# Performance work log

Measured on AMD Instinct MI355X. Metric: run time of the kernel, lower is better.

## Reference

```python
import jax, jax.numpy as jnp
import numpy as np

B, H, IN, OUT, T = 1024, 1024, 512, 8192, 15
EPS = 1e-5


def setup_inputs() -> dict:
    key = jax.random.key(0)
    ks = jax.random.split(key, 20)
    s = 0.02
    d = {
        'z': jax.random.normal(ks[0], (B, H), jnp.float32),
        'input_length': T,
        # ConvTranspose1d weights, torch layout [in, out, k] == jax 'IOH'
        'cw1': jax.random.normal(ks[1], (H, H, 3), jnp.float32) * s,
        'cb1': jax.random.normal(ks[2], (H,), jnp.float32) * s,
        'cw2': jax.random.normal(ks[3], (H, H, 3), jnp.float32) * s,
        'cb2': jax.random.normal(ks[4], (H,), jnp.float32) * s,
        'cw3': jax.random.normal(ks[5], (H, H, 3), jnp.float32) * s,
        'cb3': jax.random.normal(ks[6], (H,), jnp.float32) * s,
        # BatchNorm1d (eval mode: running stats)
        'bn1_g': jnp.ones((H,), jnp.float32), 'bn1_b': jnp.zeros((H,), jnp.float32),
        'bn1_m': jax.random.normal(ks[7], (H,), jnp.float32) * 0.1,
        'bn1_v': jax.random.uniform(ks[8], (H,), jnp.float32, 0.5, 1.5),
        'bn2_g': jnp.ones((H,), jnp.float32), 'bn2_b': jnp.zeros((H,), jnp.float32),
        'bn2_m': jax.random.normal(ks[9], (H,), jnp.float32) * 0.1,
        'bn2_v': jax.random.uniform(ks[10], (H,), jnp.float32, 0.5, 1.5),
        # GRUCell: weight_ih [3H, IN+H], weight_hh [3H, H]
        'w_ih': jax.random.normal(ks[11], (3 * H, IN + H), jnp.float32) * s,
        'w_hh': jax.random.normal(ks[12], (3 * H, H), jnp.float32) * s,
        'b_ih': jax.random.normal(ks[13], (3 * H,), jnp.float32) * s,
        'b_hh': jax.random.normal(ks[14], (3 * H,), jnp.float32) * s,
        # Linears (torch layout [out_features, in_features])
        'h2x_w': jax.random.normal(ks[15], (IN, H), jnp.float32) * s,
        'h2x_b': jax.random.normal(ks[16], (IN,), jnp.float32) * s,
        'dec2out_w': jax.random.normal(ks[17], (OUT, H), jnp.float32) * s,
        'dec2out_b': jnp.zeros((OUT,), jnp.float32),
        'out_w': jax.random.normal(ks[18], (OUT, H), jnp.float32) * s,
        'out_b': jnp.zeros((OUT,), jnp.float32),
    }
    return d


def _conv_t(x, w, b):
    # x: [B, C, L] ; torch ConvTranspose1d(k=3, s=2, pad=0): out L -> 2L+1
    y = jax.lax.conv_transpose(x, w, strides=(2,), padding='VALID',
                               dimension_numbers=('NCH', 'IOH', 'NCH'),
                               transpose_kernel=True)
    return y + b[None, :, None]


def _bn(x, g, bta, m, v):
    inv = g / jnp.sqrt(v + EPS)
    return (x - m[None, :, None]) * inv[None, :, None] + bta[None, :, None]


def reference(z, input_length, cw1, cb1, cw2, cb2, cw3, cb3,
              bn1_g, bn1_b, bn1_m, bn1_v, bn2_g, bn2_b, bn2_m, bn2_v,
              w_ih, w_hh, b_ih, b_hh, h2x_w, h2x_b,
              dec2out_w, dec2out_b, out_w, out_b):
    b = z.shape[0]
    # conv-transpose context: [B, H, 1] -> [B, H, 15]
    dec = z[:, :, None]
    dec = _bn(jax.nn.elu(_conv_t(dec, cw1, cb1)), bn1_g, bn1_b, bn1_m, bn1_v)
    dec = _bn(jax.nn.elu(_conv_t(dec, cw2, cb2)), bn2_g, bn2_b, bn2_m, bn2_v)
    dec = _conv_t(dec, cw3, cb3)
    dec_tbh = jnp.transpose(dec, (2, 0, 1))[:input_length]  # [T, B, H]

    inp0 = jnp.full((b, IN), float(OUT - 2), z.dtype)

    def step(carry, dec_t):
        h, inp = carry
        x = jnp.concatenate([inp, dec_t], axis=1)         # [B, IN+H]
        gi = x @ w_ih.T + b_ih
        gh = h @ w_hh.T + b_hh
        ir, iz, inn = jnp.split(gi, 3, axis=1)
        hr, hz, hn = jnp.split(gh, 3, axis=1)
        r = jax.nn.sigmoid(ir + hr)
        zg = jax.nn.sigmoid(iz + hz)
        n = jnp.tanh(inn + r * hn)
        h_new = (1.0 - zg) * n + zg * h
        inp_new = jax.nn.relu(h_new @ h2x_w.T + h2x_b)    # eval-mode branch
        return (h_new, inp_new), h_new

    (_, _), hs = jax.lax.scan(step, (z, inp0), dec_tbh)   # hs: [T, B, H]

    dec_flat = dec_tbh.reshape(-1, H)
    out_flat = hs.reshape(-1, H)
    dec_o = dec_flat @ dec2out_w.T + dec2out_b            # [T*B, OUT]
    output = out_flat @ out_w.T + out_b                   # [T*B, OUT]
    return output, dec_o
```

## Files before the change

kernel.cpp:

```cpp
#include <hip/hip_runtime.h>
#include <math.h>


#define HD    1024
#define BATCH 1024
#define IND   512
#define OUTD  8192
#define TSTEPS 15
#define EPSV  1e-5f

typedef unsigned short u16;
typedef __attribute__((ext_vector_type(8))) short bf16x8;
typedef __attribute__((ext_vector_type(8))) unsigned short u16x8;
typedef __attribute__((ext_vector_type(4))) unsigned short u16x4;
typedef __attribute__((ext_vector_type(4))) float f32x4;

__device__ __forceinline__ u16 f2b(float f) {
    union { float f; unsigned u; } x; x.f = f;
    unsigned r = x.u + 0x7fffu + ((x.u >> 16) & 1u);
    return (u16)(r >> 16);
}
__device__ __forceinline__ float b2f(u16 v) {
    union { unsigned u; float f; } x; x.u = ((unsigned)v) << 16; return x.f;
}

typedef __attribute__((address_space(1))) const void gas_t;
typedef __attribute__((address_space(3))) void las_t;
__device__ __forceinline__ void gload_lds16(const u16* g, u16* l) {
    __builtin_amdgcn_global_load_lds((gas_t*)g, (las_t*)l, 16, 0, 0);
}

template<int EPI, bool WF32, bool WB16>
__device__ __forceinline__ void gemm_tile128(
    u16* As, u16* Bs,
    int bm, int bn,
    int K1, const u16* A1, int lda1, const u16* B1, int ldb1,
    int K2, const u16* A2, int lda2, const u16* B2, int ldb2,
    const float* bias,
    const float* bng, const float* bnb, const float* bnm, const float* bnv,
    float* Cf, u16* Cb, int ldc)
{
    const int tid  = threadIdx.x;
    const int lane = tid & 63;
    const int w    = tid >> 6;
    const int wr   = w >> 1, wc = w & 1;
    const int r_in = lane >> 2;
    const int c_in = (lane & 3) * 8;

    f32x4 acc[4][4];
#pragma unroll
    for (int m = 0; m < 4; ++m)
#pragma unroll
        for (int n = 0; n < 4; ++n) acc[m][n] = (f32x4){0.f, 0.f, 0.f, 0.f};

#pragma unroll 1
    for (int pair = 0; pair < 2; ++pair) {
        const int K = pair ? K2 : K1;
        if (K == 0) continue;
        const int lda = pair ? lda2 : lda1;
        const int ldb = pair ? ldb2 : ldb1;
        const u16* Ag = (pair ? A2 : A1) + (size_t)bm * lda;
        const u16* Bg = (pair ? B2 : B1) + (size_t)bn * ldb;

        for (int k0 = 0; k0 < K; k0 += 32) {
#pragma unroll
            for (int i = 0; i < 2; ++i) {
                gload_lds16(Ag + (size_t)(i * 64 + w * 16 + r_in) * lda + k0 + c_in,
                            &As[i * 2048 + w * 512]);
                gload_lds16(Bg + (size_t)(i * 64 + w * 16 + r_in) * ldb + k0 + c_in,
                            &Bs[i * 2048 + w * 512]);
            }
            __syncthreads();

            const int fr = lane & 15;
            const int fk = (lane >> 4) * 8;
            bf16x8 av[4], bv[4];
#pragma unroll
            for (int m = 0; m < 4; ++m)
                av[m] = *(const bf16x8*)&As[(wr * 64 + m * 16 + fr) * 32 + fk];
#pragma unroll
            for (int n = 0; n < 4; ++n)
                bv[n] = *(const bf16x8*)&Bs[(wc * 64 + n * 16 + fr) * 32 + fk];
#pragma unroll
            for (int m = 0; m < 4; ++m)
#pragma unroll
                for (int n = 0; n < 4; ++n)
                    acc[m][n] = __builtin_amdgcn_mfma_f32_16x16x32_bf16(
                                    av[m], bv[n], acc[m][n], 0, 0, 0);
            __syncthreads();
        }
    }

    const int col_l = lane & 15;
    const int row_h = (lane >> 4) * 4;
#pragma unroll
    for (int m = 0; m < 4; ++m) {
#pragma unroll
        for (int j = 0; j < 4; ++j) {
            const int row = bm + wr * 64 + m * 16 + row_h + j;
#pragma unroll
            for (int n = 0; n < 4; ++n) {
                const int col = bn + wc * 64 + n * 16 + col_l;
                float v = acc[m][n][j] + bias[col];
                if (EPI == 1) {
                    float e = v > 0.f ? v : expm1f(v);
                    float sc = bng[col] * rsqrtf(bnv[col] + EPSV);
                    v = (e - bnm[col]) * sc + bnb[col];
                }
                if (WF32) Cf[(size_t)row * ldc + col] = v;
                if (WB16) Cb[(size_t)row * ldc + col] = f2b(v);
            }
        }
    }
}

__device__ __forceinline__ void proj_rider(u16* sm, int g,
    const u16* A, const u16* B, const float* bias, float* C)
{
    gemm_tile128<0, true, false>(sm, sm + 4096,
        (g >> 6) * 128, (g & 63) * 128,
        HD, A, HD, B, HD, 0, nullptr, 0, nullptr, 0,
        bias, nullptr, nullptr, nullptr, nullptr, C, nullptr, OUTD);
}

template<int EPI>
__launch_bounds__(256)
__global__ void conv_gemm(int Lin, const u16* X, const u16* W, const float* bias,
                          const float* bng, const float* bnb, const float* bnm, const float* bnv,
                          u16* Y)
{
    __shared__ __align__(16) u16 sm[8192];
    const int t = blockIdx.z;
    int l0 = 0, k0 = 0, l1 = 0, k1 = 0, cnt = 0;
    for (int l = 0; l < Lin; ++l) {
        int k = t - 2 * l;
        if (k >= 0 && k < 3) { if (!cnt) { l0 = l; k0 = k; } else { l1 = l; k1 = k; } ++cnt; }
    }
    const size_t BH = (size_t)BATCH * HD, HH = (size_t)HD * HD;
    gemm_tile128<EPI, false, true>(sm, sm + 4096,
        blockIdx.y * 128, blockIdx.x * 128,
        HD, X + l0 * BH, HD, W + k0 * HH, HD,
        cnt > 1 ? HD : 0, X + l1 * BH, HD, W + k1 * HH, HD,
        bias, bng, bnb, bnm, bnv, nullptr, Y + (size_t)t * BH, HD);
}

__launch_bounds__(512, 2)
__global__ void gemm256(int nbn, int nk,
    const u16* __restrict__ A, const u16* __restrict__ B,
    const float* __restrict__ bias, u16* __restrict__ Cb,
    int lda, int ldb, int ldc)
{
    const int nwg = gridDim.x;
    const int q = nwg >> 3, r = nwg & 7;
    const int xcd = blockIdx.x & 7, idx = blockIdx.x >> 3;
    const int wg = (xcd < r ? xcd * (q + 1) : r * (q + 1) + (xcd - r) * q) + idx;
    int bm, bn;
    const int nbm = nwg / nbn;
    if ((nbn & 3) == 0 && (nbm & 1) == 0) {
        const int nsc = nbn >> 2;
        const int super = wg >> 3, inner = wg & 7;
        const int sr = super / nsc, sc = super - sr * nsc;
        bm = (sr * 2 + (inner >> 2)) * 256;
        bn = (sc * 4 + (inner & 3)) * 256;
    } else {
        bm = (wg / nbn) * 256;
        bn = (wg % nbn) * 256;
    }

    __shared__ __align__(16) u16 smem[2][2][256 * 64];
    u16 (*As)[256 * 64] = smem[0];
    u16 (*Bs)[256 * 64] = smem[1];

    const int tid = threadIdx.x;
    const int w = tid >> 6, l = tid & 63;
    const int wr = w >> 2, wc = w & 3;
    const int srow = l >> 3;
    const int scb  = (l & 7) ^ srow;
    const int fr = l & 15, fcb = l >> 4, swz = l & 7;

    const u16* Ag = A + (size_t)bm * lda;
    const u16* Bg = B + (size_t)bn * ldb;

    auto stage = [&](int b, int kt) {
        const int k0 = kt * 64 + scb * 8;
#pragma unroll
        for (int rr = 0; rr < 4; ++rr)
            gload_lds16(Ag + (size_t)(rr * 64 + w * 8 + srow) * lda + k0,
                        &As[b][(rr * 64 + w * 8) * 64]);
#pragma unroll
        for (int rr = 0; rr < 4; ++rr)
            gload_lds16(Bg + (size_t)(rr * 64 + w * 8 + srow) * ldb + k0,
                        &Bs[b][(rr * 64 + w * 8) * 64]);
    };

    f32x4 acc[8][4];
#pragma unroll
    for (int m = 0; m < 8; ++m)
#pragma unroll
        for (int n = 0; n < 4; ++n) acc[m][n] = (f32x4){0.f, 0.f, 0.f, 0.f};

    stage(0, 0);
    asm volatile("s_waitcnt vmcnt(0)" ::: "memory");
    asm volatile("s_barrier" ::: "memory");

    for (int kt = 0; kt < nk; ++kt) {
        const int c = kt & 1;
        if (kt + 1 < nk) stage(c ^ 1, kt + 1);
#pragma unroll
        for (int ks = 0; ks < 2; ++ks) {
            bf16x8 av[8], bv[4];
#pragma unroll
            for (int m = 0; m < 8; ++m)
                av[m] = *(const bf16x8*)&As[c][
                    (wr * 128 + m * 16 + fr) * 64 + (((ks * 4 + fcb) ^ swz) * 8)];
#pragma unroll
            for (int n = 0; n < 4; ++n)
                bv[n] = *(const bf16x8*)&Bs[c][
                    (wc * 64 + n * 16 + fr) * 64 + (((ks * 4 + fcb) ^ swz) * 8)];
            __builtin_amdgcn_s_setprio(1);
#pragma unroll
            for (int m = 0; m < 8; ++m)
#pragma unroll
                for (int n = 0; n < 4; ++n)
                    acc[m][n] = __builtin_amdgcn_mfma_f32_16x16x32_bf16(
                                    av[m], bv[n], acc[m][n], 0, 0, 0);
            __builtin_amdgcn_s_setprio(0);
        }
        asm volatile("s_waitcnt vmcnt(0)" ::: "memory");
        asm volatile("s_barrier" ::: "memory");
    }

    float* fsm = (float*)smem;
    const int row_h = (l >> 4) * 4;
#pragma unroll 1
    for (int hh = 0; hh < 2; ++hh) {
        __syncthreads();
        if (wr == hh) {
#pragma unroll
            for (int m = 0; m < 8; ++m)
#pragma unroll
                for (int j = 0; j < 4; ++j) {
                    const int rl = m * 16 + row_h + j;
#pragma unroll
                    for (int n = 0; n < 4; ++n)
                        fsm[rl * 256 + wc * 64 + n * 16 + fr] = acc[m][n][j];
                }
        }
        __syncthreads();
#pragma unroll
        for (int it = 0; it < 16; ++it) {
            const int fid = it * 512 + tid;
            const int rl = fid >> 6;
            const int cf = (fid & 63) * 4;
            float4 v = *(const float4*)&fsm[rl * 256 + cf];
            v.x += bias[bn + cf + 0];
            v.y += bias[bn + cf + 1];
            v.z += bias[bn + cf + 2];
            v.w += bias[bn + cf + 3];
            u16x4 o;
            o[0] = f2b(v.x); o[1] = f2b(v.y); o[2] = f2b(v.z); o[3] = f2b(v.w);
            *(u16x4*)&Cb[(size_t)(bm + hh * 128 + rl) * ldc + bn + cf] = o;
        }
    }
}

#define KTILE(Ag, lda_, Bg, ldb_, k0_, ACC2)                                      \
  {                                                                               \
    const int k0 = (k0_);                                                         \
    gload_lds16((Ag) + (size_t)(tid >> 2) * (lda_) + k0 + (tid & 3) * 8,          \
                &As[tid * 8]);                                                    \
    _Pragma("unroll")                                                             \
    for (int i_ = 0; i_ < 3; ++i_) {                                              \
      const int u_ = tid + i_ * 256;                                              \
      gload_lds16((Bg) + (size_t)((u_ >> 8) * HD + bn + ((u_ & 255) >> 2)) * (ldb_)\
                       + k0 + (u_ & 3) * 8,                                       \
                  &Bs[u_ * 8]);                                                   \
    }                                                                             \
    __syncthreads();                                                              \
    {                                                                             \
      bf16x8 av0 = *(const bf16x8*)&As[(wr * 32 + fr) * 32 + fk];                 \
      bf16x8 av1 = *(const bf16x8*)&As[(wr * 32 + 16 + fr) * 32 + fk];            \
      _Pragma("unroll")                                                           \
      for (int n_ = 0; n_ < 2; ++n_) {                                            \
        const int bo = (wc * 32 + n_ * 16 + fr) * 32 + fk;                        \
        bf16x8 bv = *(const bf16x8*)&Bs[bo];                                      \
        ar[0][n_] = __builtin_amdgcn_mfma_f32_16x16x32_bf16(av0, bv, ar[0][n_], 0, 0, 0); \
        ar[1][n_] = __builtin_amdgcn_mfma_f32_16x16x32_bf16(av1, bv, ar[1][n_], 0, 0, 0); \
        bv = *(const bf16x8*)&Bs[2048 + bo];                                      \
        az[0][n_] = __builtin_amdgcn_mfma_f32_16x16x32_bf16(av0, bv, az[0][n_], 0, 0, 0); \
        az[1][n_] = __builtin_amdgcn_mfma_f32_16x16x32_bf16(av1, bv, az[1][n_], 0, 0, 0); \
        bv = *(const bf16x8*)&Bs[4096 + bo];                                      \
        ACC2[0][n_] = __builtin_amdgcn_mfma_f32_16x16x32_bf16(av0, bv, ACC2[0][n_], 0, 0, 0); \
        ACC2[1][n_] = __builtin_amdgcn_mfma_f32_16x16x32_bf16(av1, bv, ACC2[1][n_], 0, 0, 0); \
      }                                                                           \
    }                                                                             \
    __syncthreads();                                                              \
  }

__launch_bounds__(256)
__global__ void gih_cell(int t,
    const u16* __restrict__ inpb,  const u16* __restrict__ wih,
    const u16* __restrict__ hbp,   const u16* __restrict__ whh,
    const u16* __restrict__ gdect, const float* __restrict__ extra0,
    const float* __restrict__ b_hh, const float* __restrict__ hp,
    float* __restrict__ hf, u16* __restrict__ hsbt,
    const u16* __restrict__ dec3b, const u16* __restrict__ d2owb,
    const float* __restrict__ d2ob, float* __restrict__ out1)
{
    __shared__ __align__(16) u16 sm[8192];
    const int bid = blockIdx.x;
    const int tid = threadIdx.x, l = tid & 63, w = tid >> 6;
    const int wr = w >> 1, wc = w & 1;
    const int fr = l & 15, fk = (l >> 4) * 8;

    if (bid >= 256) {
        proj_rider(sm, t * 512 + (bid - 256), dec3b, d2owb, d2ob, out1);
        return;
    }

    u16* As = sm;
    u16* Bs = sm + 2048;
    const int bm = (bid >> 4) * 64;
    const int bn = (bid & 15) * 64;

    f32x4 ar[2][2], az[2][2], ain[2][2], ahn[2][2];
#pragma unroll
    for (int m = 0; m < 2; ++m)
#pragma unroll
        for (int n = 0; n < 2; ++n) {
            ar[m][n] = (f32x4){0.f, 0.f, 0.f, 0.f};
            az[m][n] = (f32x4){0.f, 0.f, 0.f, 0.f};
            ain[m][n] = (f32x4){0.f, 0.f, 0.f, 0.f};
            ahn[m][n] = (f32x4){0.f, 0.f, 0.f, 0.f};
        }

    const u16* Ah = hbp + (size_t)bm * HD;
    const u16* Ai = inpb + (size_t)bm * IND;
    for (int kt = 0; kt < 32; ++kt)
        KTILE(Ah, HD, whh, HD, kt * 32, ahn);
    if (t > 0)
        for (int kt = 0; kt < 16; ++kt)
            KTILE(Ai, IND, wih, (IND + HD), kt * 32, ain);

    const int rh = (l >> 4) * 4;
#pragma unroll
    for (int m = 0; m < 2; ++m)
#pragma unroll
        for (int n = 0; n < 2; ++n)
#pragma unroll
            for (int j = 0; j < 4; ++j) {
                const int R = bm + wr * 32 + m * 16 + rh + j;
                const int C = bn + wc * 32 + n * 16 + fr;
                const size_t g3 = (size_t)R * (3 * HD);
                float gr  = ar[m][n][j] + b2f(gdect[g3 + C])      + b_hh[C];
                float gz  = az[m][n][j] + b2f(gdect[g3 + HD + C]) + b_hh[HD + C];
                float gin = ain[m][n][j] + b2f(gdect[g3 + 2 * HD + C]);
                float ghn = ahn[m][n][j] + b_hh[2 * HD + C];
                if (extra0) {
                    gr  += extra0[C];
                    gz  += extra0[HD + C];
                    gin += extra0[2 * HD + C];
                }
                const float rg = 1.f / (1.f + expf(-gr));
                const float zg = 1.f / (1.f + expf(-gz));
                const float nn = tanhf(gin + rg * ghn);
                const float h  = (1.f - zg) * nn + zg * hp[(size_t)R * HD + C];
                hf[(size_t)R * HD + C] = h;
                hsbt[(size_t)R * HD + C] = f2b(h);
            }
}

__launch_bounds__(256)
__global__ void h2x_k(int t,
    const u16* __restrict__ hbp, const u16* __restrict__ wx,
    const float* __restrict__ xb, u16* __restrict__ inp,
    const u16* __restrict__ hsb, const u16* __restrict__ outwb,
    const float* __restrict__ outb, float* __restrict__ out0)
{
    __shared__ __align__(16) u16 sm[8192];
    const int bid = blockIdx.x;
    const int tid = threadIdx.x, l = tid & 63, w = tid >> 6;
    const int wr = w >> 1, wc = w & 1;
    const int fr = l & 15, fk = (l >> 4) * 8;

    if (bid >= 128) {
        proj_rider(sm, (t - 1) * 512 + (bid - 128), hsb, outwb, outb, out0);
        return;
    }

    u16* As = sm;
    u16* Bs = sm + 2048;
    const int bm = (bid >> 3) * 64;
    const int bn = (bid & 7) * 64;

    f32x4 acc[2][2];
#pragma unroll
    for (int m = 0; m < 2; ++m)
#pragma unroll
        for (int n = 0; n < 2; ++n) acc[m][n] = (f32x4){0.f, 0.f, 0.f, 0.f};
    const u16* Ag = hbp + (size_t)bm * HD;
    const u16* Bg = wx + (size_t)bn * HD;
    for (int kt = 0; kt < 32; ++kt) {
        const int k0 = kt * 32;
        gload_lds16(Ag + (size_t)(tid >> 2) * HD + k0 + (tid & 3) * 8, &As[tid * 8]);
        gload_lds16(Bg + (size_t)(tid >> 2) * HD + k0 + (tid & 3) * 8, &Bs[tid * 8]);
        __syncthreads();
        bf16x8 av0 = *(const bf16x8*)&As[(wr * 32 + fr) * 32 + fk];
        bf16x8 av1 = *(const bf16x8*)&As[(wr * 32 + 16 + fr) * 32 + fk];
#pragma unroll
        for (int n = 0; n < 2; ++n) {
            bf16x8 bv = *(const bf16x8*)&Bs[(wc * 32 + n * 16 + fr) * 32 + fk];
            acc[0][n] = __builtin_amdgcn_mfma_f32_16x16x32_bf16(av0, bv, acc[0][n], 0, 0, 0);
            acc[1][n] = __builtin_amdgcn_mfma_f32_16x16x32_bf16(av1, bv, acc[1][n], 0, 0, 0);
        }
        __syncthreads();
    }
    const int rh = (l >> 4) * 4;
#pragma unroll
    for (int m = 0; m < 2; ++m)
#pragma unroll
        for (int n = 0; n < 2; ++n)
#pragma unroll
            for (int j = 0; j < 4; ++j) {
                const int R = bm + wr * 32 + m * 16 + rh + j;
                const int C = bn + wc * 32 + n * 16 + fr;
                inp[(size_t)R * IND + C] = f2b(fmaxf(acc[m][n][j] + xb[C], 0.f));
            }
}

__launch_bounds__(256)
__global__ void proj_k(int g0, const u16* __restrict__ A, const u16* __restrict__ B,
                       const float* __restrict__ bias, float* __restrict__ C)
{
    __shared__ __align__(16) u16 sm[8192];
    proj_rider(sm, g0 + blockIdx.x, A, B, bias, C);
}

__global__ void pack_w3(const float* __restrict__ c1, const float* __restrict__ c2,
                        const float* __restrict__ c3, u16* __restrict__ p1,
                        u16* __restrict__ p2, u16* __restrict__ p3)
{
    __shared__ float lds[768];
    const float* cw = blockIdx.y == 0 ? c1 : (blockIdx.y == 1 ? c2 : c3);
    u16* wp = blockIdx.y == 0 ? p1 : (blockIdx.y == 1 ? p2 : p3);
    const int o = blockIdx.x, t = threadIdx.x;
    const float* src = cw + (size_t)o * (HD * 3);
    for (int i0 = 0; i0 < HD; i0 += 256) {
#pragma unroll
        for (int r = 0; r < 3; ++r) lds[t + 256 * r] = src[i0 * 3 + t + 256 * r];
        __syncthreads();
#pragma unroll
        for (int k = 0; k < 3; ++k)
            wp[(size_t)k * HD * HD + (size_t)o * HD + i0 + t] = f2b(lds[t * 3 + k]);
        __syncthreads();
    }
}

__global__ void cvt_all(const float* s0, u16* d0, int n0,
                        const float* s1, u16* d1, int n1,
                        const float* s2, u16* d2, int n2,
                        const float* s3, u16* d3, int n3,
                        const float* s4, u16* d4, int n4,
                        const float* s5, u16* d5, int n5)
{
    const float* s; u16* d; int n;
    switch (blockIdx.y) {
        case 0:  s = s0; d = d0; n = n0; break;
        case 1:  s = s1; d = d1; n = n1; break;
        case 2:  s = s2; d = d2; n = n2; break;
        case 3:  s = s3; d = d3; n = n3; break;
        case 4:  s = s4; d = d4; n = n4; break;
        default: s = s5; d = d5; n = n5; break;
    }
    int i = (blockIdx.x * 256 + threadIdx.x) * 8;
    if (i >= n) return;
    float4 a = *(const float4*)(s + i);
    float4 b = *(const float4*)(s + i + 4);
    u16x8 o;
    o[0] = f2b(a.x); o[1] = f2b(a.y); o[2] = f2b(a.z); o[3] = f2b(a.w);
    o[4] = f2b(b.x); o[5] = f2b(b.y); o[6] = f2b(b.z); o[7] = f2b(b.w);
    *(u16x8*)(d + i) = o;
}

__global__ void ext0_k(const float* __restrict__ w_ih, float* __restrict__ e0)
{
    const int j = blockIdx.x, lane = threadIdx.x;
    float s = 0.f;
    for (int k = lane; k < IND; k += 64) s += w_ih[(size_t)j * (IND + HD) + k];
    for (int off = 32; off; off >>= 1) s += __shfl_down(s, off);
    if (lane == 0) e0[j] = 8190.f * s;
}

extern "C" void kernel_launch(void* const* d_in, const int* in_sizes, int n_in,
                              void* d_out, int out_size, void* d_ws, size_t ws_size,
                              hipStream_t stream)
{
    (void)in_sizes; (void)n_in; (void)out_size; (void)ws_size;

    const float* z    = (const float*)d_in[0];
    const float* cw1  = (const float*)d_in[2];
    const float* cb1  = (const float*)d_in[3];
    const float* cw2  = (const float*)d_in[4];
    const float* cb2  = (const float*)d_in[5];
    const float* cw3  = (const float*)d_in[6];
    const float* cb3  = (const float*)d_in[7];
    const float* bn1g = (const float*)d_in[8];
    const float* bn1b = (const float*)d_in[9];
    const float* bn1m = (const float*)d_in[10];
    const float* bn1v = (const float*)d_in[11];
    const float* bn2g = (const float*)d_in[12];
    const float* bn2b = (const float*)d_in[13];
    const float* bn2m = (const float*)d_in[14];
    const float* bn2v = (const float*)d_in[15];
    const float* w_ih = (const float*)d_in[16];
    const float* w_hh = (const float*)d_in[17];
    const float* b_ih = (const float*)d_in[18];
    const float* b_hh = (const float*)d_in[19];
    const float* h2xw = (const float*)d_in[20];
    const float* h2xb = (const float*)d_in[21];
    const float* d2ow = (const float*)d_in[22];
    const float* d2ob = (const float*)d_in[23];
    const float* outw = (const float*)d_in[24];
    const float* outb = (const float*)d_in[25];

    const size_t HH = (size_t)HD * HD, BH = (size_t)BATCH * HD;
    const size_t B3H = (size_t)BATCH * 3 * HD;

    u16* wsb = (u16*)d_ws;
    size_t off = 0;
    auto A16 = [&](size_t n) { u16* p = wsb + off; off += n; return p; };
    u16* wp1   = A16(3 * HH);
    u16* wp2   = A16(3 * HH);
    u16* wp3   = A16(3 * HH);
    u16* wihb  = A16((size_t)3 * HD * (IND + HD));
    u16* whhb  = A16(3 * HH);
    u16* h2xbw = A16((size_t)IND * HD);
    u16* outwb = A16((size_t)OUTD * HD);
    u16* d2owb = A16((size_t)OUTD * HD);
    u16* zb    = A16(BH);
    u16* decab = A16(3 * BH);
    u16* decbb = A16(7 * BH);
    u16* dec3b = A16(15 * BH);
    u16* hsb   = A16(15 * BH);
    u16* inpb  = A16((size_t)BATCH * IND);
    u16* gdecb = A16((size_t)TSTEPS * B3H);
    float* wsf = (float*)(wsb + ((off + 1) & ~(size_t)1));
    size_t foff = 0;
    auto A32 = [&](size_t n) { float* p = wsf + foff; foff += n; return p; };
    float* h0f   = A32(BH);
    float* h1f   = A32(BH);
    float* extra0= A32(3 * HD);

    pack_w3<<<dim3(HD, 3), 256, 0, stream>>>(cw1, cw2, cw3, wp1, wp2, wp3);
    cvt_all<<<dim3(4096, 6), 256, 0, stream>>>(
        z, zb, (int)BH,
        w_ih, wihb, 3 * HD * (IND + HD),
        w_hh, whhb, (int)(3 * HH),
        h2xw, h2xbw, IND * HD,
        outw, outwb, OUTD * HD,
        d2ow, d2owb, OUTD * HD);
    ext0_k<<<3 * HD, 64, 0, stream>>>(w_ih, extra0);

    conv_gemm<1><<<dim3(8, 8, 3), 256, 0, stream>>>(1, zb, wp1, cb1,
        bn1g, bn1b, bn1m, bn1v, decab);
    conv_gemm<1><<<dim3(8, 8, 7), 256, 0, stream>>>(3, decab, wp2, cb2,
        bn2g, bn2b, bn2m, bn2v, decbb);
    conv_gemm<0><<<dim3(8, 8, 15), 256, 0, stream>>>(7, decbb, wp3, cb3,
        nullptr, nullptr, nullptr, nullptr, dec3b);

    gemm256<<<dim3((TSTEPS * BATCH / 256) * (3 * HD / 256)), 512, 0, stream>>>(
        3 * HD / 256, HD / 64,
        dec3b, wihb + IND, b_ih, gdecb, HD, IND + HD, 3 * HD);

    float* out0 = (float*)d_out;
    float* out1 = out0 + (size_t)TSTEPS * BATCH * OUTD;
    for (int t = 0; t < TSTEPS; ++t) {
        const u16* hbp   = t ? hsb + (size_t)(t - 1) * BH : zb;
        const float* hpf = (t == 0) ? z : (((t - 1) & 1) ? h1f : h0f);
        float* hwf = (t & 1) ? h1f : h0f;
        if (t > 0)
            h2x_k<<<640, 256, 0, stream>>>(t, hbp, h2xbw, h2xb, inpb,
                hsb, outwb, outb, out0);
        gih_cell<<<768, 256, 0, stream>>>(t,
            inpb, wihb, hbp, whhb, gdecb + (size_t)t * B3H,
            t ? nullptr : extra0, b_hh, hpf, hwf, hsb + (size_t)t * BH,
            dec3b, d2owb, d2ob, out1);
    }
    proj_k<<<512, 256, 0, stream>>>(14 * 512, hsb, outwb, outb, out0);
}
```

Baseline: 1.514 ms.

## Shrink per-step projection riders and finish projections in one 256-tile GEMM

Halves the output-projection tiles that ride along with each recurrent-step kernel, going from 512 to 256 tiles per step. The remaining rows of both output projections (dec2out and out) go to a new 256x256-tile proj256 kernel launched after the scan. That kernel reuses the gemm256 main loop, which is factored into a shared body. The aim is to shorten the serial per-step kernels and run the leftover bulk GEMM work with higher-efficiency large tiles. The cost is less overlap of projection work with the latency-bound recurrence, plus one large tail kernel.

After: 1.691 ms. +11.7%, slower.

```diff
diff --git a/kernel.cpp b/kernel.cpp
--- a/kernel.cpp
+++ b/kernel.cpp
@@ -142,6 +142,76 @@
         HD, X + l0 * BH, HD, W + k0 * HH, HD,
         cnt > 1 ? HD : 0, X + l1 * BH, HD, W + k1 * HH, HD,
         bias, bng, bnb, bnm, bnv, nullptr, Y + (size_t)t * BH, HD);
+}
+
+struct G256 {
+    f32x4 acc[8][4];
+};
+
+__device__ __forceinline__ void gemm256_body(u16* smem_, G256& g,
+    int bm, int bn, int nk,
+    const u16* __restrict__ A, const u16* __restrict__ B, int lda, int ldb)
+{
+    u16 (*As)[256 * 64] = (u16(*)[256 * 64])smem_;
+    u16 (*Bs)[256 * 64] = (u16(*)[256 * 64])(smem_ + 2 * 256 * 64);
+
+    const int tid = threadIdx.x;
+    const int w = tid >> 6, l = tid & 63;
+    const int wr = w >> 2, wc = w & 3;
+    const int srow = l >> 3;
+    const int scb  = (l & 7) ^ srow;
+    const int fr = l & 15, fcb = l >> 4, swz = l & 7;
+
+    const u16* Ag = A + (size_t)bm * lda;
+    const u16* Bg = B + (size_t)bn * ldb;
+
+    auto stage = [&](int b, int kt) {
+        const int k0 = kt * 64 + scb * 8;
+#pragma unroll
+        for (int rr = 0; rr < 4; ++rr)
+            gload_lds16(Ag + (size_t)(rr * 64 + w * 8 + srow) * lda + k0,
+                        &As[b][(rr * 64 + w * 8) * 64]);
+#pragma unroll
+        for (int rr = 0; rr < 4; ++rr)
+            gload_lds16(Bg + (size_t)(rr * 64 + w * 8 + srow) * ldb + k0,
+                        &Bs[b][(rr * 64 + w * 8) * 64]);
+    };
+
+#pragma unroll
+    for (int m = 0; m < 8; ++m)
+#pragma unroll
+        for (int n = 0; n < 4; ++n) g.acc[m][n] = (f32x4){0.f, 0.f, 0.f, 0.f};
+
+    stage(0, 0);
+    asm volatile("s_waitcnt vmcnt(0)" ::: "memory");
+    asm volatile("s_barrier" ::: "memory");
+
+    for (int kt = 0; kt < nk; ++kt) {
+        const int c = kt & 1;
+        if (kt + 1 < nk) stage(c ^ 1, kt + 1);
+#pragma unroll
+        for (int ks = 0; ks < 2; ++ks) {
+            bf16x8 av[8], bv[4];
+#pragma unroll
+            for (int m = 0; m < 8; ++m)
+                av[m] = *(const bf16x8*)&As[c][
+                    (wr * 128 + m * 16 + fr) * 64 + (((ks * 4 + fcb) ^ swz) * 8)];
+#pragma unroll
+            for (int n = 0; n < 4; ++n)
+                bv[n] = *(const bf16x8*)&Bs[c][
+                    (wc * 64 + n * 16 + fr) * 64 + (((ks * 4 + fcb) ^ swz) * 8)];
+            __builtin_amdgcn_s_setprio(1);
+#pragma unroll
+            for (int m = 0; m < 8; ++m)
+#pragma unroll
+                for (int n = 0; n < 4; ++n)
+                    g.acc[m][n] = __builtin_amdgcn_mfma_f32_16x16x32_bf16(
+                                    av[m], bv[n], g.acc[m][n], 0, 0, 0);
+            __builtin_amdgcn_s_setprio(0);
+        }
+        asm volatile("s_waitcnt vmcnt(0)" ::: "memory");
+        asm volatile("s_barrier" ::: "memory");
+    }
 }
 
 __launch_bounds__(512, 2)
@@ -167,69 +237,14 @@
         bn = (wg % nbn) * 256;
     }
 
-    __shared__ __align__(16) u16 smem[2][2][256 * 64];
-    u16 (*As)[256 * 64] = smem[0];
-    u16 (*Bs)[256 * 64] = smem[1];
+    __shared__ __align__(16) u16 smem[4 * 256 * 64];
+    G256 g;
+    gemm256_body(smem, g, bm, bn, nk, A, B, lda, ldb);
 
     const int tid = threadIdx.x;
     const int w = tid >> 6, l = tid & 63;
     const int wr = w >> 2, wc = w & 3;
-    const int srow = l >> 3;
-    const int scb  = (l & 7) ^ srow;
-    const int fr = l & 15, fcb = l >> 4, swz = l & 7;
-
-    const u16* Ag = A + (size_t)bm * lda;
-    const u16* Bg = B + (size_t)bn * ldb;
-
-    auto stage = [&](int b, int kt) {
-        const int k0 = kt * 64 + scb * 8;
-#pragma unroll
-        for (int rr = 0; rr < 4; ++rr)
-            gload_lds16(Ag + (size_t)(rr * 64 + w * 8 + srow) * lda + k0,
-                        &As[b][(rr * 64 + w * 8) * 64]);
-#pragma unroll
-        for (int rr = 0; rr < 4; ++rr)
-            gload_lds16(Bg + (size_t)(rr * 64 + w * 8 + srow) * ldb + k0,
-                        &Bs[b][(rr * 64 + w * 8) * 64]);
-    };
-
-    f32x4 acc[8][4];
-#pragma unroll
-    for (int m = 0; m < 8; ++m)
-#pragma unroll
-        for (int n = 0; n < 4; ++n) acc[m][n] = (f32x4){0.f, 0.f, 0.f, 0.f};
-
-    stage(0, 0);
-    asm volatile("s_waitcnt vmcnt(0)" ::: "memory");
-    asm volatile("s_barrier" ::: "memory");
-
-    for (int kt = 0; kt < nk; ++kt) {
-        const int c = kt & 1;
-        if (kt + 1 < nk) stage(c ^ 1, kt + 1);
-#pragma unroll
-        for (int ks = 0; ks < 2; ++ks) {
-            bf16x8 av[8], bv[4];
-#pragma unroll
-            for (int m = 0; m < 8; ++m)
-                av[m] = *(const bf16x8*)&As[c][
-                    (wr * 128 + m * 16 + fr) * 64 + (((ks * 4 + fcb) ^ swz) * 8)];
-#pragma unroll
-            for (int n = 0; n < 4; ++n)
-                bv[n] = *(const bf16x8*)&Bs[c][
-                    (wc * 64 + n * 16 + fr) * 64 + (((ks * 4 + fcb) ^ swz) * 8)];
-            __builtin_amdgcn_s_setprio(1);
-#pragma unroll
-            for (int m = 0; m < 8; ++m)
-#pragma unroll
-                for (int n = 0; n < 4; ++n)
-                    acc[m][n] = __builtin_amdgcn_mfma_f32_16x16x32_bf16(
-                                    av[m], bv[n], acc[m][n], 0, 0, 0);
-            __builtin_amdgcn_s_setprio(0);
-        }
-        asm volatile("s_waitcnt vmcnt(0)" ::: "memory");
-        asm volatile("s_barrier" ::: "memory");
-    }
-
+    const int fr = l & 15;
     float* fsm = (float*)smem;
     const int row_h = (l >> 4) * 4;
 #pragma unroll 1
@@ -243,7 +258,7 @@
                     const int rl = m * 16 + row_h + j;
 #pragma unroll
                     for (int n = 0; n < 4; ++n)
-                        fsm[rl * 256 + wc * 64 + n * 16 + fr] = acc[m][n][j];
+                        fsm[rl * 256 + wc * 64 + n * 16 + fr] = g.acc[m][n][j];
                 }
         }
         __syncthreads();
@@ -260,6 +275,75 @@
             u16x4 o;
             o[0] = f2b(v.x); o[1] = f2b(v.y); o[2] = f2b(v.z); o[3] = f2b(v.w);
             *(u16x4*)&Cb[(size_t)(bm + hh * 128 + rl) * ldc + bn + cf] = o;
+        }
+    }
+}
+
+__launch_bounds__(512, 2)
+__global__ void proj256(
+    const u16* __restrict__ Adec, const u16* __restrict__ Bd2o,
+    const float* __restrict__ d2ob, float* __restrict__ out1,
+    const u16* __restrict__ Ahs, const u16* __restrict__ Bout,
+    const float* __restrict__ outb, float* __restrict__ out0)
+{
+    const int nwg = gridDim.x;
+    const int q = nwg >> 3, r = nwg & 7;
+    const int xcd = blockIdx.x & 7, idx = blockIdx.x >> 3;
+    const int wg = (xcd < r ? xcd * (q + 1) : r * (q + 1) + (xcd - r) * q) + idx;
+
+    const u16 *A, *B; const float* bias; float* C;
+    int bm, bn;
+    if (wg < 960) {
+        const int super = wg >> 3, inner = wg & 7;
+        const int sr = super >> 3, sc = super & 7;
+        bm = 7680 + (sr * 2 + (inner >> 2)) * 256;
+        bn = (sc * 4 + (inner & 3)) * 256;
+        A = Adec; B = Bd2o; bias = d2ob; C = out1;
+    } else {
+        const int w2 = wg - 960;
+        const int super = w2 >> 3, inner = w2 & 7;
+        const int sr = super >> 3, sc = super & 7;
+        bm = 7168 + (sr * 2 + (inner >> 2)) * 256;
+        bn = (sc * 4 + (inner & 3)) * 256;
+        A = Ahs; B = Bout; bias = outb; C = out0;
+    }
+
+    __shared__ __align__(16) u16 smem[4 * 256 * 64];
+    G256 g;
+    gemm256_body(smem, g, bm, bn, HD / 64, A, B, HD, HD);
+
+    const int tid = threadIdx.x;
+    const int w = tid >> 6, l = tid & 63;
+    const int wr = w >> 2, wc = w & 3;
+    const int fr = l & 15;
+    float* fsm = (float*)smem;
+    const int row_h = (l >> 4) * 4;
+#pragma unroll 1
+    for (int hh = 0; hh < 2; ++hh) {
+        __syncthreads();
+        if (wr == hh) {
+#pragma unroll
+            for (int m = 0; m < 8; ++m)
+#pragma unroll
+                for (int j = 0; j < 4; ++j) {
+                    const int rl = m * 16 + row_h + j;
+#pragma unroll
+                    for (int n = 0; n < 4; ++n)
+                        fsm[rl * 256 + wc * 64 + n * 16 + fr] = g.acc[m][n][j];
+                }
+        }
+        __syncthreads();
+#pragma unroll
+        for (int it = 0; it < 16; ++it) {
+            const int fid = it * 512 + tid;
+            const int rl = fid >> 6;
+            const int cf = (fid & 63) * 4;
+            float4 v = *(const float4*)&fsm[rl * 256 + cf];
+            v.x += bias[bn + cf + 0];
+            v.y += bias[bn + cf + 1];
+            v.z += bias[bn + cf + 2];
+            v.w += bias[bn + cf + 3];
+            *(float4*)&C[(size_t)(bm + hh * 128 + rl) * OUTD + bn + cf] = v;
         }
     }
 }
@@ -314,7 +398,7 @@
     const int fr = l & 15, fk = (l >> 4) * 8;
 
     if (bid >= 256) {
-        proj_rider(sm, t * 512 + (bid - 256), dec3b, d2owb, d2ob, out1);
+        proj_rider(sm, t * 256 + (bid - 256), dec3b, d2owb, d2ob, out1);
         return;
     }
 
@@ -384,7 +468,7 @@
     const int fr = l & 15, fk = (l >> 4) * 8;
 
     if (bid >= 128) {
-        proj_rider(sm, (t - 1) * 512 + (bid - 128), hsb, outwb, outb, out0);
+        proj_rider(sm, (t - 1) * 256 + (bid - 128), hsb, outwb, outb, out0);
         return;
     }
 
@@ -426,14 +510,6 @@
                 const int C = bn + wc * 32 + n * 16 + fr;
                 inp[(size_t)R * IND + C] = f2b(fmaxf(acc[m][n][j] + xb[C], 0.f));
             }
-}
-
-__launch_bounds__(256)
-__global__ void proj_k(int g0, const u16* __restrict__ A, const u16* __restrict__ B,
-                       const float* __restrict__ bias, float* __restrict__ C)
-{
-    __shared__ __align__(16) u16 sm[8192];
-    proj_rider(sm, g0 + blockIdx.x, A, B, bias, C);
 }
 
 __global__ void pack_w3(const float* __restrict__ c1, const float* __restrict__ c2,
@@ -579,12 +655,13 @@
         const float* hpf = (t == 0) ? z : (((t - 1) & 1) ? h1f : h0f);
         float* hwf = (t & 1) ? h1f : h0f;
         if (t > 0)
-            h2x_k<<<640, 256, 0, stream>>>(t, hbp, h2xbw, h2xb, inpb,
+            h2x_k<<<384, 256, 0, stream>>>(t, hbp, h2xbw, h2xb, inpb,
                 hsb, outwb, outb, out0);
-        gih_cell<<<768, 256, 0, stream>>>(t,
+        gih_cell<<<512, 256, 0, stream>>>(t,
             inpb, wihb, hbp, whhb, gdecb + (size_t)t * B3H,
             t ? nullptr : extra0, b_hh, hpf, hwf, hsb + (size_t)t * BH,
             dec3b, d2owb, d2ob, out1);
     }
-    proj_k<<<512, 256, 0, stream>>>(14 * 512, hsb, outwb, outb, out0);
-}
+    proj256<<<1984, 512, 0, stream>>>(dec3b, d2owb, d2ob, out1,
+                                      hsb, outwb, outb, out0);
+}
```

## Spread decoder input-gate GEMM across recurrent steps as rider blocks

Applied to the files above, without the earlier changes.

Removes the upfront large gemm256 that computed the decoder-input gate projections for all 15 timesteps. A small head kernel now computes the projections for steps 0 and 1, and each later gih_cell launch (t ≤ 12) carries 192 extra rider blocks that compute the step t+2 slice with the 128-tile GEMM. The aim is to fill idle CUs during the latency-bound recurrent steps instead of paying for a separate GEMM. In exchange the work runs on a less efficient 128 tile path and adds load to the recurrent kernels, which could lengthen the critical path.

Measured after the change: 1.486 ms, median of 2. Within noise of the previous version (-1.8%).

```diff
diff --git a/kernel.cpp b/kernel.cpp
--- a/kernel.cpp
+++ b/kernel.cpp
@@ -123,6 +123,28 @@
         bias, nullptr, nullptr, nullptr, nullptr, C, nullptr, OUTD);
 }
 
+__device__ __forceinline__ void gdec_rider(u16* sm, int t, int g,
+    const u16* dec3b, const u16* wihb, const float* b_ih, u16* gdecb)
+{
+    const int row = g / 24, col = g - row * 24;
+    gemm_tile128<0, false, true>(sm, sm + 4096,
+        row * 128, col * 128,
+        HD, dec3b + (size_t)t * BATCH * HD, HD, wihb + IND, IND + HD,
+        0, nullptr, 0, nullptr, 0,
+        b_ih, nullptr, nullptr, nullptr, nullptr,
+        nullptr, gdecb + (size_t)t * BATCH * 3 * HD, 3 * HD);
+}
+
+__launch_bounds__(256)
+__global__ void gdec_head(const u16* __restrict__ dec3b, const u16* __restrict__ wihb,
+                          const float* __restrict__ b_ih, u16* __restrict__ gdecb)
+{
+    __shared__ __align__(16) u16 sm[8192];
+    const int bid = blockIdx.x;
+    if (bid < 192) gdec_rider(sm, 0, bid, dec3b, wihb, b_ih, gdecb);
+    else           gdec_rider(sm, 1, bid - 192, dec3b, wihb, b_ih, gdecb);
+}
+
 template<int EPI>
 __launch_bounds__(256)
 __global__ void conv_gemm(int Lin, const u16* X, const u16* W, const float* bias,
@@ -142,126 +164,6 @@
         HD, X + l0 * BH, HD, W + k0 * HH, HD,
         cnt > 1 ? HD : 0, X + l1 * BH, HD, W + k1 * HH, HD,
         bias, bng, bnb, bnm, bnv, nullptr, Y + (size_t)t * BH, HD);
-}
-
-__launch_bounds__(512, 2)
-__global__ void gemm256(int nbn, int nk,
-    const u16* __restrict__ A, const u16* __restrict__ B,
-    const float* __restrict__ bias, u16* __restrict__ Cb,
-    int lda, int ldb, int ldc)
-{
-    const int nwg = gridDim.x;
-    const int q = nwg >> 3, r = nwg & 7;
-    const int xcd = blockIdx.x & 7, idx = blockIdx.x >> 3;
-    const int wg = (xcd < r ? xcd * (q + 1) : r * (q + 1) + (xcd - r) * q) + idx;
-    int bm, bn;
-    const int nbm = nwg / nbn;
-    if ((nbn & 3) == 0 && (nbm & 1) == 0) {
-        const int nsc = nbn >> 2;
-        const int super = wg >> 3, inner = wg & 7;
-        const int sr = super / nsc, sc = super - sr * nsc;
-        bm = (sr * 2 + (inner >> 2)) * 256;
-        bn = (sc * 4 + (inner & 3)) * 256;
-    } else {
-        bm = (wg / nbn) * 256;
-        bn = (wg % nbn) * 256;
-    }
-
-    __shared__ __align__(16) u16 smem[2][2][256 * 64];
-    u16 (*As)[256 * 64] = smem[0];
-    u16 (*Bs)[256 * 64] = smem[1];
-
-    const int tid = threadIdx.x;
-    const int w = tid >> 6, l = tid & 63;
-    const int wr = w >> 2, wc = w & 3;
-    const int srow = l >> 3;
-    const int scb  = (l & 7) ^ srow;
-    const int fr = l & 15, fcb = l >> 4, swz = l & 7;
-
-    const u16* Ag = A + (size_t)bm * lda;
-    const u16* Bg = B + (size_t)bn * ldb;
-
-    auto stage = [&](int b, int kt) {
-        const int k0 = kt * 64 + scb * 8;
-#pragma unroll
-        for (int rr = 0; rr < 4; ++rr)
-            gload_lds16(Ag + (size_t)(rr * 64 + w * 8 + srow) * lda + k0,
-                        &As[b][(rr * 64 + w * 8) * 64]);
-#pragma unroll
-        for (int rr = 0; rr < 4; ++rr)
-            gload_lds16(Bg + (size_t)(rr * 64 + w * 8 + srow) * ldb + k0,
-                        &Bs[b][(rr * 64 + w * 8) * 64]);
-    };
-
-    f32x4 acc[8][4];
-#pragma unroll
-    for (int m = 0; m < 8; ++m)
-#pragma unroll
-        for (int n = 0; n < 4; ++n) acc[m][n] = (f32x4){0.f, 0.f, 0.f, 0.f};
-
-    stage(0, 0);
-    asm volatile("s_waitcnt vmcnt(0)" ::: "memory");
-    asm volatile("s_barrier" ::: "memory");
-
-    for (int kt = 0; kt < nk; ++kt) {
-        const int c = kt & 1;
-        if (kt + 1 < nk) stage(c ^ 1, kt + 1);
-#pragma unroll
-        for (int ks = 0; ks < 2; ++ks) {
-            bf16x8 av[8], bv[4];
-#pragma unroll
-            for (int m = 0; m < 8; ++m)
-                av[m] = *(const bf16x8*)&As[c][
-                    (wr * 128 + m * 16 + fr) * 64 + (((ks * 4 + fcb) ^ swz) * 8)];
-#pragma unroll
-            for (int n = 0; n < 4; ++n)
-                bv[n] = *(const bf16x8*)&Bs[c][
-                    (wc * 64 + n * 16 + fr) * 64 + (((ks * 4 + fcb) ^ swz) * 8)];
-            __builtin_amdgcn_s_setprio(1);
-#pragma unroll
-            for (int m = 0; m < 8; ++m)
-#pragma unroll
-                for (int n = 0; n < 4; ++n)
-                    acc[m][n] = __builtin_amdgcn_mfma_f32_16x16x32_bf16(
-                                    av[m], bv[n], acc[m][n], 0, 0, 0);
-            __builtin_amdgcn_s_setprio(0);
-        }
-        asm volatile("s_waitcnt vmcnt(0)" ::: "memory");
-        asm volatile("s_barrier" ::: "memory");
-    }
-
-    float* fsm = (float*)smem;
-    const int row_h = (l >> 4) * 4;
-#pragma unroll 1
-    for (int hh = 0; hh < 2; ++hh) {
-        __syncthreads();
-        if (wr == hh) {
-#pragma unroll
-            for (int m = 0; m < 8; ++m)
-#pragma unroll
-                for (int j = 0; j < 4; ++j) {
-                    const int rl = m * 16 + row_h + j;
-#pragma unroll
-                    for (int n = 0; n < 4; ++n)
-                        fsm[rl * 256 + wc * 64 + n * 16 + fr] = acc[m][n][j];
-                }
-        }
-        __syncthreads();
-#pragma unroll
-        for (int it = 0; it < 16; ++it) {
-            const int fid = it * 512 + tid;
-            const int rl = fid >> 6;
-            const int cf = (fid & 63) * 4;
-            float4 v = *(const float4*)&fsm[rl * 256 + cf];
-            v.x += bias[bn + cf + 0];
-            v.y += bias[bn + cf + 1];
-            v.z += bias[bn + cf + 2];
-            v.w += bias[bn + cf + 3];
-            u16x4 o;
-            o[0] = f2b(v.x); o[1] = f2b(v.y); o[2] = f2b(v.z); o[3] = f2b(v.w);
-            *(u16x4*)&Cb[(size_t)(bm + hh * 128 + rl) * ldc + bn + cf] = o;
-        }
-    }
 }
 
 #define KTILE(Ag, lda_, Bg, ldb_, k0_, ACC2)                                      \
@@ -301,11 +203,12 @@
 __global__ void gih_cell(int t,
     const u16* __restrict__ inpb,  const u16* __restrict__ wih,
     const u16* __restrict__ hbp,   const u16* __restrict__ whh,
-    const u16* __restrict__ gdect, const float* __restrict__ extra0,
+    const u16* __restrict__ gdecb, const float* __restrict__ extra0,
     const float* __restrict__ b_hh, const float* __restrict__ hp,
     float* __restrict__ hf, u16* __restrict__ hsbt,
     const u16* __restrict__ dec3b, const u16* __restrict__ d2owb,
-    const float* __restrict__ d2ob, float* __restrict__ out1)
+    const float* __restrict__ d2ob, float* __restrict__ out1,
+    const float* __restrict__ b_ih)
 {
     __shared__ __align__(16) u16 sm[8192];
     const int bid = blockIdx.x;
@@ -314,7 +217,15 @@
     const int fr = l & 15, fk = (l >> 4) * 8;
 
     if (bid >= 256) {
-        proj_rider(sm, t * 512 + (bid - 256), dec3b, d2owb, d2ob, out1);
+        int rid = bid - 256;
+        if (t <= 12) {
+            if (rid < 192) {
+                gdec_rider(sm, t + 2, rid, dec3b, wih, b_ih, (u16*)gdecb);
+                return;
+            }
+            rid -= 192;
+        }
+        proj_rider(sm, t * 512 + rid, dec3b, d2owb, d2ob, out1);
         return;
     }
 
@@ -342,6 +253,7 @@
         for (int kt = 0; kt < 16; ++kt)
             KTILE(Ai, IND, wih, (IND + HD), kt * 32, ain);
 
+    const u16* gdect = gdecb + (size_t)t * BATCH * 3 * HD;
     const int rh = (l >> 4) * 4;
 #pragma unroll
     for (int m = 0; m < 2; ++m)
@@ -568,9 +480,7 @@
     conv_gemm<0><<<dim3(8, 8, 15), 256, 0, stream>>>(7, decbb, wp3, cb3,
         nullptr, nullptr, nullptr, nullptr, dec3b);
 
-    gemm256<<<dim3((TSTEPS * BATCH / 256) * (3 * HD / 256)), 512, 0, stream>>>(
-        3 * HD / 256, HD / 64,
-        dec3b, wihb + IND, b_ih, gdecb, HD, IND + HD, 3 * HD);
+    gdec_head<<<384, 256, 0, stream>>>(dec3b, wihb, b_ih, gdecb);
 
     float* out0 = (float*)d_out;
     float* out1 = out0 + (size_t)TSTEPS * BATCH * OUTD;
@@ -581,10 +491,11 @@
         if (t > 0)
             h2x_k<<<640, 256, 0, stream>>>(t, hbp, h2xbw, h2xb, inpb,
                 hsb, outwb, outb, out0);
-        gih_cell<<<768, 256, 0, stream>>>(t,
-            inpb, wihb, hbp, whhb, gdecb + (size_t)t * B3H,
+        const int ggrid = (t <= 12) ? 960 : 768;
+        gih_cell<<<ggrid, 256, 0, stream>>>(t,
+            inpb, wihb, hbp, whhb, gdecb,
             t ? nullptr : extra0, b_hh, hpf, hwf, hsb + (size_t)t * BH,
-            dec3b, d2owb, d2ob, out1);
+            dec3b, d2owb, d2ob, out1, b_ih);
     }
     proj_k<<<512, 256, 0, stream>>>(14 * 512, hsb, outwb, outb, out0);
 }
```
